# Kernel optimization log

Hardware: AMD Instinct MI355X
Metric: run time of the kernel (lower is better)

Reference implementation:

```python
import jax, jax.numpy as jnp
import numpy as np

GAMMA = 1.4
EPS = 1e-6
N_NEWTON = 20
B, K, NT, NX = 16, 64, 128, 256


def _sound_speed(rho, p):
    return jnp.sqrt(jnp.clip(GAMMA * p / jnp.clip(rho, EPS), EPS))


def setup_inputs() -> dict:
    key = jax.random.key(0)
    k1, k2, k3, k4, k5, k6 = jax.random.split(key, 6)
    xs = jnp.sort(jax.random.uniform(k1, (B, K + 1), dtype=jnp.float32), axis=1)
    ks = jax.random.uniform(k2, (B, K), dtype=jnp.float32, minval=0.1, maxval=1.1)
    ks_v = jax.random.normal(k3, (B, K), dtype=jnp.float32)
    ks_p = jax.random.uniform(k4, (B, K), dtype=jnp.float32, minval=0.1, maxval=1.1)
    pieces_mask = jnp.ones((B, K), dtype=jnp.float32)
    t_coords = jax.random.uniform(k5, (B, NT, NX), dtype=jnp.float32)
    x_coords = jax.random.uniform(k6, (B, NT, NX), dtype=jnp.float32)
    return {"xs": xs, "ks": ks, "ks_v": ks_v, "ks_p": ks_p,
            "pieces_mask": pieces_mask, "t_coords": t_coords, "x_coords": x_coords}


def reference(xs, ks, ks_v, ks_p, pieces_mask, t_coords, x_coords):
    gm1 = GAMMA - 1.0
    gp1 = GAMMA + 1.0
    exp_rare = gm1 / (2.0 * GAMMA)

    # left/right states at the K-1 interfaces: (B, K-1)
    rho_L, rho_R = ks[:, :-1], ks[:, 1:]
    u_L, u_R = ks_v[:, :-1], ks_v[:, 1:]
    p_L, p_R = ks_p[:, :-1], ks_p[:, 1:]

    c_L = _sound_speed(rho_L, p_L)
    c_R = _sound_speed(rho_R, p_R)
    A_L = 2.0 / (gp1 * jnp.clip(rho_L, EPS))
    A_R = 2.0 / (gp1 * jnp.clip(rho_R, EPS))
    B_L = gm1 / gp1 * p_L
    B_R = gm1 / gp1 * p_R

    def wave_f_df(p, p_K, A_K, B_K, c_K):
        denom = jnp.clip(p + B_K, EPS)
        sqrt_AoD = jnp.sqrt(jnp.clip(A_K / denom, EPS))
        f_shock = (p - p_K) * sqrt_AoD
        df_shock = sqrt_AoD * (1.0 - (p - p_K) / (2.0 * denom))
        p_ratio = jnp.clip(p / jnp.clip(p_K, EPS), EPS)
        f_rare = 2.0 * c_K / gm1 * (p_ratio ** exp_rare - 1.0)
        df_rare = c_K / (GAMMA * jnp.clip(p_K, EPS)) * p_ratio ** (-gp1 / (2.0 * GAMMA))
        is_shock = p > p_K
        return jnp.where(is_shock, f_shock, f_rare), jnp.where(is_shock, df_shock, df_rare)

    # two-rarefaction initial guess
    p0 = jnp.clip(((c_L + c_R - gm1 / 2.0 * (u_R - u_L)) /
                   (c_L / jnp.clip(p_L, EPS) ** exp_rare +
                    c_R / jnp.clip(p_R, EPS) ** exp_rare)) ** (1.0 / exp_rare), EPS)

    def newton_step(i, p_star):
        f_L, df_L = wave_f_df(p_star, p_L, A_L, B_L, c_L)
        f_R, df_R = wave_f_df(p_star, p_R, A_R, B_R, c_R)
        residual = f_L + f_R + (u_R - u_L)
        jacobian = jnp.clip(df_L + df_R, EPS)
        return jnp.clip(p_star - residual / jacobian, EPS)

    p_star = jax.lax.fori_loop(0, N_NEWTON, newton_step, p0)

    f_L, _ = wave_f_df(p_star, p_L, A_L, B_L, c_L)
    f_R, _ = wave_f_df(p_star, p_R, A_R, B_R, c_R)
    u_star = 0.5 * (u_L + u_R) + 0.5 * (f_R - f_L)  # computed as in source (unused downstream)

    gp1_o_2g = gp1 / (2.0 * GAMMA)
    sigma_1 = u_L - c_L * jnp.sqrt(jnp.clip(1.0 + gp1_o_2g * (p_star / jnp.clip(p_L, EPS) - 1.0), EPS))
    speed_left = jnp.where(p_star > p_L, sigma_1, u_L - c_L)
    sigma_3 = u_R + c_R * jnp.sqrt(jnp.clip(1.0 + gp1_o_2g * (p_star / jnp.clip(p_R, EPS) - 1.0), EPS))
    speed_right = jnp.where(p_star > p_R, sigma_3, u_R + c_R)

    x_d = xs[:, 1:K][:, None, None, :]           # (B,1,1,K-1)
    sr = speed_right[:, None, None, :]
    sl = speed_left[:, None, None, :]
    xi = (x_coords[..., None] - x_d) / (t_coords[..., None] + EPS)  # (B,nt,nx,K-1)

    penalty_left_seg = jax.nn.relu(xi - sr)
    penalty_right_seg = jax.nn.relu(sl - xi)
    pad_last = ((0, 0), (0, 0), (0, 0), (0, 1))
    pad_first = ((0, 0), (0, 0), (0, 0), (1, 0))
    bias = -(jnp.pad(penalty_left_seg, pad_last) + jnp.pad(penalty_right_seg, pad_first))

    mask = pieces_mask[:, None, None, :]
    bias = bias * mask + (mask == 0).astype(bias.dtype) * (-1e9)
    return bias
```

## Files before the change

### kernel.cpp

```cpp
#include <hip/hip_runtime.h>
#include <math.h>

#define GAMMA_F 1.4f
#define EPS_F 1e-6f
#define B_ 16
#define K_ 64
#define NT_ 128
#define NX_ 256
#define NI 63
#define N_NEWTON 20

__device__ __forceinline__ void wave_f_df(float p, float p_K, float A_K, float B_K,
                                          float c_K, float& f, float& df) {
    const float gm1 = GAMMA_F - 1.0f;
    const float gp1 = GAMMA_F + 1.0f;
    const float exp_rare = gm1 / (2.0f * GAMMA_F);
    float denom = fmaxf(p + B_K, EPS_F);
    float sqrt_AoD = sqrtf(fmaxf(A_K / denom, EPS_F));
    float f_shock = (p - p_K) * sqrt_AoD;
    float df_shock = sqrt_AoD * (1.0f - (p - p_K) / (2.0f * denom));
    float pKc = fmaxf(p_K, EPS_F);
    float p_ratio = fmaxf(p / pKc, EPS_F);
    float f_rare = 2.0f * c_K / gm1 * (powf(p_ratio, exp_rare) - 1.0f);
    float df_rare = c_K / (GAMMA_F * pKc) * powf(p_ratio, -gp1 / (2.0f * GAMMA_F));
    bool is_shock = p > p_K;
    f = is_shock ? f_shock : f_rare;
    df = is_shock ? df_shock : df_rare;
}

__global__ void riemann_solve_kernel(const float* __restrict__ xs,
                                     const float* __restrict__ ks,
                                     const float* __restrict__ ks_v,
                                     const float* __restrict__ ks_p,
                                     float* __restrict__ sr_ws,
                                     float* __restrict__ sl_ws,
                                     float* __restrict__ xd_ws) {
    const int b = blockIdx.x;
    const int i = threadIdx.x;
    if (i >= NI) return;

    const float gm1 = GAMMA_F - 1.0f;
    const float gp1 = GAMMA_F + 1.0f;
    const float exp_rare = gm1 / (2.0f * GAMMA_F);

    const int base = b * K_ + i;
    float rho_L = ks[base],     rho_R = ks[base + 1];
    float u_L   = ks_v[base],   u_R   = ks_v[base + 1];
    float p_L   = ks_p[base],   p_R   = ks_p[base + 1];

    float c_L = sqrtf(fmaxf(GAMMA_F * p_L / fmaxf(rho_L, EPS_F), EPS_F));
    float c_R = sqrtf(fmaxf(GAMMA_F * p_R / fmaxf(rho_R, EPS_F), EPS_F));
    float A_L = 2.0f / (gp1 * fmaxf(rho_L, EPS_F));
    float A_R = 2.0f / (gp1 * fmaxf(rho_R, EPS_F));
    float B_L = gm1 / gp1 * p_L;
    float B_R = gm1 / gp1 * p_R;

    float num = c_L + c_R - 0.5f * gm1 * (u_R - u_L);
    float den = c_L / powf(fmaxf(p_L, EPS_F), exp_rare)
              + c_R / powf(fmaxf(p_R, EPS_F), exp_rare);
    float p_star = fmaxf(powf(num / den, 1.0f / exp_rare), EPS_F);

    #pragma unroll 1
    for (int it = 0; it < N_NEWTON; ++it) {
        float fL, dfL, fR, dfR;
        wave_f_df(p_star, p_L, A_L, B_L, c_L, fL, dfL);
        wave_f_df(p_star, p_R, A_R, B_R, c_R, fR, dfR);
        float residual = fL + fR + (u_R - u_L);
        float jac = fmaxf(dfL + dfR, EPS_F);
        p_star = fmaxf(p_star - residual / jac, EPS_F);
    }

    const float gp1_o_2g = gp1 / (2.0f * GAMMA_F);
    float s1 = u_L - c_L * sqrtf(fmaxf(1.0f + gp1_o_2g * (p_star / fmaxf(p_L, EPS_F) - 1.0f), EPS_F));
    float speed_left = (p_star > p_L) ? s1 : (u_L - c_L);
    float s3 = u_R + c_R * sqrtf(fmaxf(1.0f + gp1_o_2g * (p_star / fmaxf(p_R, EPS_F) - 1.0f), EPS_F));
    float speed_right = (p_star > p_R) ? s3 : (u_R + c_R);

    sl_ws[base] = speed_left;
    sr_ws[base] = speed_right;
    xd_ws[base] = xs[b * (K_ + 1) + i + 1];
}

__global__ __launch_bounds__(256) void
bias_kernel(const float* __restrict__ t_coords,
            const float* __restrict__ x_coords,
            const float* __restrict__ pieces_mask,
            const float* __restrict__ sr_ws,
            const float* __restrict__ sl_ws,
            const float* __restrict__ xd_ws,
            float* __restrict__ out) {
    __shared__ float s_sr[NI];
    __shared__ float s_sl[NI];
    __shared__ float s_xd[NI];
    __shared__ float s_mask[K_];

    const int bid = blockIdx.x;
    const int b = bid >> 11;
    const int blk_in_b = bid & 2047;
    const int tid = threadIdx.x;

    {
        const int g = tid >> 6;
        const int r = tid & 63;
        if (g == 0) { if (r < NI) s_sr[r] = sr_ws[b * K_ + r]; }
        else if (g == 1) { if (r < NI) s_sl[r] = sl_ws[b * K_ + r]; }
        else if (g == 2) { if (r < NI) s_xd[r] = xd_ws[b * K_ + r]; }
        else { s_mask[r] = pieces_mask[b * K_ + r]; }
    }
    __syncthreads();

    const int p_local = tid >> 4;
    const int j = tid & 15;
    const int pt = (blk_in_b << 4) + p_local;
    const long long pbase = (long long)b * (NT_ * NX_) + pt;

    const float t = t_coords[pbase];
    const float x = x_coords[pbase];
    const float inv_t = 1.0f / (t + EPS_F);

    const int k0 = j << 2;
    float res[4];
    #pragma unroll
    for (int q = 0; q < 4; ++q) {
        const int k = k0 + q;
        float pl = 0.0f, pr = 0.0f;
        if (k < NI) {
            float xi = (x - s_xd[k]) * inv_t;
            pl = fmaxf(xi - s_sr[k], 0.0f);
        }
        if (k >= 1) {
            float xi = (x - s_xd[k - 1]) * inv_t;
            pr = fmaxf(s_sl[k - 1] - xi, 0.0f);
        }
        float bias = -(pl + pr);
        float m = s_mask[k];
        res[q] = bias * m + ((m == 0.0f) ? -1.0e9f : 0.0f);
    }

    float4* outv = reinterpret_cast<float4*>(out + pbase * K_ + k0);
    *outv = make_float4(res[0], res[1], res[2], res[3]);
}

extern "C" void kernel_launch(void* const* d_in, const int* in_sizes, int n_in,
                              void* d_out, int out_size, void* d_ws, size_t ws_size,
                              hipStream_t stream) {
    const float* xs          = (const float*)d_in[0];
    const float* ks          = (const float*)d_in[1];
    const float* ks_v        = (const float*)d_in[2];
    const float* ks_p        = (const float*)d_in[3];
    const float* pieces_mask = (const float*)d_in[4];
    const float* t_coords    = (const float*)d_in[5];
    const float* x_coords    = (const float*)d_in[6];
    float* out = (float*)d_out;

    float* ws = (float*)d_ws;
    float* sr_ws = ws;
    float* sl_ws = ws + B_ * K_;
    float* xd_ws = ws + 2 * B_ * K_;

    riemann_solve_kernel<<<B_, 64, 0, stream>>>(xs, ks, ks_v, ks_p, sr_ws, sl_ws, xd_ws);

    const int blocks = B_ * (NT_ * NX_ / 16);
    bias_kernel<<<blocks, 256, 0, stream>>>(t_coords, x_coords, pieces_mask,
                                            sr_ws, sl_ws, xd_ws, out);
}
```

Measured before the change: 194.4 us.

## Process multiple points per block with register-cached params and nontemporal stores

The bias kernel now handles 8 groups of 16 points per block instead of one. Per-interface parameters (xd, sr, sl, mask) are loaded once into registers and reused across iterations. Output is written with nontemporal vector stores, and boundary handling uses sentinel values instead of branches. The Newton solver reuses one powf to get the rarefaction derivative, which changes rounding slightly. Fewer blocks means less shared-memory setup and sync overhead per point, at the cost of less parallelism per launch.

```diff
diff --git a/kernel.cpp b/kernel.cpp
--- a/kernel.cpp
+++ b/kernel.cpp
@@ -10,10 +10,16 @@
 #define NI 63
 #define N_NEWTON 20
 
+#define PTS_PER_ITER 16
+#define ITERS 8
+#define PTS_PER_BLOCK (PTS_PER_ITER * ITERS)
+#define BLOCKS_PER_B (NT_ * NX_ / PTS_PER_BLOCK)
+
+typedef float floatx4 __attribute__((ext_vector_type(4)));
+
 __device__ __forceinline__ void wave_f_df(float p, float p_K, float A_K, float B_K,
                                           float c_K, float& f, float& df) {
     const float gm1 = GAMMA_F - 1.0f;
-    const float gp1 = GAMMA_F + 1.0f;
     const float exp_rare = gm1 / (2.0f * GAMMA_F);
     float denom = fmaxf(p + B_K, EPS_F);
     float sqrt_AoD = sqrtf(fmaxf(A_K / denom, EPS_F));
@@ -21,8 +27,9 @@
     float df_shock = sqrt_AoD * (1.0f - (p - p_K) / (2.0f * denom));
     float pKc = fmaxf(p_K, EPS_F);
     float p_ratio = fmaxf(p / pKc, EPS_F);
-    float f_rare = 2.0f * c_K / gm1 * (powf(p_ratio, exp_rare) - 1.0f);
-    float df_rare = c_K / (GAMMA_F * pKc) * powf(p_ratio, -gp1 / (2.0f * GAMMA_F));
+    float pre = powf(p_ratio, exp_rare);
+    float f_rare = 2.0f * c_K / gm1 * (pre - 1.0f);
+    float df_rare = c_K / (GAMMA_F * pKc) * (pre / p_ratio);
     bool is_shock = p > p_K;
     f = is_shock ? f_shock : f_rare;
     df = is_shock ? df_shock : df_rare;
@@ -47,6 +54,7 @@
     float rho_L = ks[base],     rho_R = ks[base + 1];
     float u_L   = ks_v[base],   u_R   = ks_v[base + 1];
     float p_L   = ks_p[base],   p_R   = ks_p[base + 1];
+    const float du = u_R - u_L;
 
     float c_L = sqrtf(fmaxf(GAMMA_F * p_L / fmaxf(rho_L, EPS_F), EPS_F));
     float c_R = sqrtf(fmaxf(GAMMA_F * p_R / fmaxf(rho_R, EPS_F), EPS_F));
@@ -55,7 +63,7 @@
     float B_L = gm1 / gp1 * p_L;
     float B_R = gm1 / gp1 * p_R;
 
-    float num = c_L + c_R - 0.5f * gm1 * (u_R - u_L);
+    float num = c_L + c_R - 0.5f * gm1 * du;
     float den = c_L / powf(fmaxf(p_L, EPS_F), exp_rare)
               + c_R / powf(fmaxf(p_R, EPS_F), exp_rare);
     float p_star = fmaxf(powf(num / den, 1.0f / exp_rare), EPS_F);
@@ -65,7 +73,7 @@
         float fL, dfL, fR, dfR;
         wave_f_df(p_star, p_L, A_L, B_L, c_L, fL, dfL);
         wave_f_df(p_star, p_R, A_R, B_R, c_R, fR, dfR);
-        float residual = fL + fR + (u_R - u_L);
+        float residual = fL + fR + du;
         float jac = fmaxf(dfL + dfR, EPS_F);
         p_star = fmaxf(p_star - residual / jac, EPS_F);
     }
@@ -95,8 +103,8 @@
     __shared__ float s_mask[K_];
 
     const int bid = blockIdx.x;
-    const int b = bid >> 11;
-    const int blk_in_b = bid & 2047;
+    const int b = bid >> 8;
+    const int blk_in_b = bid & 255;
     const int tid = threadIdx.x;
 
     {
@@ -111,34 +119,64 @@
 
     const int p_local = tid >> 4;
     const int j = tid & 15;
-    const int pt = (blk_in_b << 4) + p_local;
-    const long long pbase = (long long)b * (NT_ * NX_) + pt;
-
-    const float t = t_coords[pbase];
-    const float x = x_coords[pbase];
-    const float inv_t = 1.0f / (t + EPS_F);
-
     const int k0 = j << 2;
-    float res[4];
+
+    float xdr[5];
+    #pragma unroll
+    for (int q = -1; q <= 3; ++q) {
+        int k = k0 + q;
+        xdr[q + 1] = (k >= 0 && k < NI) ? s_xd[k] : 0.0f;
+    }
+    float srr[4], slr[4], mkr[4], madd[4];
     #pragma unroll
     for (int q = 0; q < 4; ++q) {
-        const int k = k0 + q;
-        float pl = 0.0f, pr = 0.0f;
-        if (k < NI) {
-            float xi = (x - s_xd[k]) * inv_t;
-            pl = fmaxf(xi - s_sr[k], 0.0f);
+        int k = k0 + q;
+        srr[q] = (k < NI) ? s_sr[k] : 3.0e38f;
+        slr[q] = (k >= 1) ? s_sl[k - 1] : -3.0e38f;
+        float m = s_mask[k];
+        mkr[q] = m;
+        madd[q] = (m == 0.0f) ? -1.0e9f : 0.0f;
+    }
+
+    const int pt0 = blk_in_b * PTS_PER_BLOCK + p_local;
+    const long long bbase = (long long)b * (NT_ * NX_);
+    const float* tp = t_coords + bbase + pt0;
+    const float* xp = x_coords + bbase + pt0;
+    float* op = out + (bbase + pt0) * (long long)K_ + k0;
+
+    #pragma unroll
+    for (int it = 0; it < ITERS; ++it) {
+        const float t = tp[it * PTS_PER_ITER];
+        const float x = xp[it * PTS_PER_ITER];
+        const float inv_t = 1.0f / (t + EPS_F);
+
+        float xi[5];
+        #pragma unroll
+        for (int q = 0; q < 5; ++q)
+            xi[q] = (x - xdr[q]) * inv_t;
+
+        float r0, r1, r2, r3;
+        {
+            float pl, pr;
+            pl = fmaxf(xi[1] - srr[0], 0.0f);
+            pr = fmaxf(slr[0] - xi[0], 0.0f);
+            r0 = -(pl + pr) * mkr[0] + madd[0];
+            pl = fmaxf(xi[2] - srr[1], 0.0f);
+            pr = fmaxf(slr[1] - xi[1], 0.0f);
+            r1 = -(pl + pr) * mkr[1] + madd[1];
+            pl = fmaxf(xi[3] - srr[2], 0.0f);
+            pr = fmaxf(slr[2] - xi[2], 0.0f);
+            r2 = -(pl + pr) * mkr[2] + madd[2];
+            pl = fmaxf(xi[4] - srr[3], 0.0f);
+            pr = fmaxf(slr[3] - xi[3], 0.0f);
+            r3 = -(pl + pr) * mkr[3] + madd[3];
         }
-        if (k >= 1) {
-            float xi = (x - s_xd[k - 1]) * inv_t;
-            pr = fmaxf(s_sl[k - 1] - xi, 0.0f);
-        }
-        float bias = -(pl + pr);
-        float m = s_mask[k];
-        res[q] = bias * m + ((m == 0.0f) ? -1.0e9f : 0.0f);
-    }
-
-    float4* outv = reinterpret_cast<float4*>(out + pbase * K_ + k0);
-    *outv = make_float4(res[0], res[1], res[2], res[3]);
+
+        floatx4 v;
+        v.x = r0; v.y = r1; v.z = r2; v.w = r3;
+        __builtin_nontemporal_store(v, reinterpret_cast<floatx4*>(op));
+        op += PTS_PER_ITER * K_;
+    }
 }
 
 extern "C" void kernel_launch(void* const* d_in, const int* in_sizes, int n_in,
@@ -160,7 +198,7 @@
 
     riemann_solve_kernel<<<B_, 64, 0, stream>>>(xs, ks, ks_v, ks_p, sr_ws, sl_ws, xd_ws);
 
-    const int blocks = B_ * (NT_ * NX_ / 16);
+    const int blocks = B_ * BLOCKS_PER_B;
     bias_kernel<<<blocks, 256, 0, stream>>>(t_coords, x_coords, pieces_mask,
                                             sr_ws, sl_ws, xd_ws, out);
 }
```

New measurement: 176.4 us. 9.3% less time.
